# Kernel tuning notes

Hardware: AMD Instinct MI355X
Metric: run time of the kernel (lower is better)

The kernel has to match this reference:

```python
import jax, jax.numpy as jnp
import numpy as np

DIM = 1024
HEADS = 16
DH = DIM // HEADS          # 64
SEQ_LEN = 4096
LATENT = 1024
HIST = SEQ_LEN - LATENT    # 3072
LN_EPS = 1e-5


def setup_inputs() -> dict:
    key = jax.random.key(0)
    ks = jax.random.split(key, 5)
    b = 2
    x = jax.random.normal(ks[0], (b, SEQ_LEN, DIM), dtype=jnp.float32)
    s = 0.02
    Wq = jax.random.normal(ks[1], (DIM, DIM), dtype=jnp.float32) * s
    Wkv = jax.random.normal(ks[2], (DIM, DIM), dtype=jnp.float32) * s
    Wo = jax.random.normal(ks[3], (DIM, DIM), dtype=jnp.float32) * s
    bo = jnp.zeros((DIM,), dtype=jnp.float32)
    gamma = jnp.ones((DH,), dtype=jnp.float32)
    beta = jnp.zeros((DH,), dtype=jnp.float32)
    return {"x": x, "Wq": Wq, "Wkv": Wkv, "Wo": Wo, "bo": bo,
            "gamma": gamma, "beta": beta}


def _rotate_half(t):
    t1, t2 = jnp.split(t, 2, axis=-1)
    return jnp.concatenate([-t2, t1], axis=-1)


def reference(x, Wq, Wkv, Wo, bo, gamma, beta):
    b, n, dim = x.shape
    # projections (nn.Linear: y = x @ W.T), split heads -> (b, h, n, d)
    q = jnp.einsum('bnd,ed->bne', x, Wq).reshape(b, n, HEADS, DH).transpose(0, 2, 1, 3)
    kv = jnp.einsum('bnd,ed->bne', x, Wkv).reshape(b, n, HEADS, DH).transpose(0, 2, 1, 3)

    # layer_num == 0: queries only for the latent segment
    q = q[:, :, HIST:, :]  # (b, h, latent, d)

    # rotary embeddings: concat-style freqs over head dim
    inv_freq = 1.0 / (10000.0 ** (jnp.arange(0, DH, 2, dtype=jnp.float32) / DH))
    freqs = jnp.arange(n, dtype=jnp.float32)[:, None] * inv_freq[None, :]  # (n, DH/2)
    emb = jnp.concatenate([freqs, freqs], axis=-1)  # (n, DH)
    cos, sin = jnp.cos(emb), jnp.sin(emb)
    q = q * cos[HIST:] + _rotate_half(q) * sin[HIST:]
    kv = kv * cos + _rotate_half(kv) * sin

    q = q * (DH ** -0.5)

    # per-kv LayerNorm over head dim
    mu = kv.mean(axis=-1, keepdims=True)
    var = ((kv - mu) ** 2).mean(axis=-1, keepdims=True)
    kvn = (kv - mu) * jax.lax.rsqrt(var + LN_EPS) * gamma + beta

    attn = jnp.einsum('bhid,bhjd->bhij', q, kvn)  # (b, h, latent, n)

    # causal mask only on latent columns: col j (>= HIST) masked if j-HIST > i
    i = jnp.arange(LATENT)[:, None]
    j = jnp.arange(n)[None, :]
    mask = (j - HIST) > i  # false for history columns (j < HIST)
    neg = -jnp.finfo(attn.dtype).max
    attn = jnp.where(mask, neg, attn)

    attn = jax.nn.softmax(attn, axis=-1)
    out = jnp.einsum('bhij,bhjd->bhid', attn, kvn)  # (b, h, latent, d)
    out = out.transpose(0, 2, 1, 3).reshape(b, LATENT, dim)
    return jnp.einsum('bnd,ed->bne', out, Wo) + bo
```

## Files before the change

### kernel.cpp

```cpp
#include <hip/hip_runtime.h>
#include <hip/hip_bf16.h>
#include <cstdint>

#define DIMC 1024
#define HEADS 16
#define DHH 64
#define SEQ 4096
#define LATENT 1024
#define HISTC 3072
#define BATCH 2

typedef __attribute__((ext_vector_type(8))) __bf16 bf16x8;
typedef __attribute__((ext_vector_type(4))) float f32x4;
typedef __attribute__((ext_vector_type(16))) float f32x16;

__global__ void k_convert(const float* __restrict__ in, __bf16* __restrict__ out, int n) {
  int stride = gridDim.x * blockDim.x;
  int nc = n >> 2;
  for (int i = blockIdx.x * blockDim.x + threadIdx.x; i < nc; i += stride) {
    float4 v = reinterpret_cast<const float4*>(in)[i];
    union { __bf16 h[4]; uint64_t u; } p;
    p.h[0] = (__bf16)v.x; p.h[1] = (__bf16)v.y;
    p.h[2] = (__bf16)v.z; p.h[3] = (__bf16)v.w;
    reinterpret_cast<uint64_t*>(out)[i] = p.u;
  }
}

__global__ void k_convert3(const float* __restrict__ a, const float* __restrict__ b,
                           const float* __restrict__ c, __bf16* __restrict__ oa,
                           __bf16* __restrict__ ob, __bf16* __restrict__ oc) {
  int id = blockIdx.x;
  const float* src; __bf16* dst;
  if (id < 512) { src = a; dst = oa; }
  else if (id < 1024) { src = b; dst = ob; id -= 512; }
  else { src = c; dst = oc; id -= 1024; }
#pragma unroll
  for (int k = 0; k < 2; ++k) {
    int idx = id * 512 + k * 256 + threadIdx.x;
    float4 v = reinterpret_cast<const float4*>(src)[idx];
    union { __bf16 h[4]; uint64_t u; } p;
    p.h[0] = (__bf16)v.x; p.h[1] = (__bf16)v.y;
    p.h[2] = (__bf16)v.z; p.h[3] = (__bf16)v.w;
    reinterpret_cast<uint64_t*>(dst)[idx] = p.u;
  }
}

__device__ __forceinline__ void gload16(void* lds, const void* g) {
  __builtin_amdgcn_global_load_lds(
      (const __attribute__((address_space(1))) unsigned int*)g,
      (__attribute__((address_space(3))) unsigned int*)lds, 16, 0, 0);
}

template<int QREMAP, int BIAS>
__launch_bounds__(256)
__global__ void k_gemm(const __bf16* __restrict__ A, const __bf16* __restrict__ Bw,
                       float* __restrict__ C, const float* __restrict__ bias,
                       int M, int N, int K) {
  __shared__ __align__(16) char lds[16384];
  const int t = threadIdx.x;
  const int l = t & 63, w = t >> 6;
  const int wr = w >> 1, wc = w & 1;
  const int m0 = blockIdx.y * 128, n0 = blockIdx.x * 128;
  const int lrow = l & 15, lk = l >> 4;
  f32x4 acc[4][4] = {};

  for (int k0 = 0; k0 < K; k0 += 32) {
    if (k0) __syncthreads();
#pragma unroll
    for (int i = 0; i < 2; ++i) {
      int c = i * 256 + t;
      int row = c >> 2, kc = c & 3;
      int mi = m0 + row;
      if (QREMAP) mi += HISTC + (mi >> 10) * HISTC;
      gload16(lds + c * 16, A + (size_t)mi * K + k0 + kc * 8);
      gload16(lds + 8192 + c * 16, Bw + (size_t)(n0 + row) * K + k0 + kc * 8);
    }
    __syncthreads();
    bf16x8 af[4], bfr[4];
#pragma unroll
    for (int m = 0; m < 4; ++m)
      af[m] = *reinterpret_cast<const bf16x8*>(lds + (wr * 64 + m * 16 + lrow) * 64 + lk * 16);
#pragma unroll
    for (int n = 0; n < 4; ++n)
      bfr[n] = *reinterpret_cast<const bf16x8*>(lds + 8192 + (wc * 64 + n * 16 + lrow) * 64 + lk * 16);
#pragma unroll
    for (int m = 0; m < 4; ++m)
#pragma unroll
      for (int n = 0; n < 4; ++n)
        acc[m][n] = __builtin_amdgcn_mfma_f32_16x16x32_bf16(af[m], bfr[n], acc[m][n], 0, 0, 0);
  }

#pragma unroll
  for (int m = 0; m < 4; ++m)
#pragma unroll
    for (int n = 0; n < 4; ++n)
#pragma unroll
      for (int r = 0; r < 4; ++r) {
        int row = m0 + wr * 64 + m * 16 + (l >> 4) * 4 + r;
        int col = n0 + wc * 64 + n * 16 + (l & 15);
        float v = acc[m][n][r];
        if (BIAS) v += bias[col];
        C[(size_t)row * N + col] = v;
      }
}

__launch_bounds__(256)
__global__ void k_gemmqkv(const __bf16* __restrict__ x16,
                          const __bf16* __restrict__ wkv16,
                          const __bf16* __restrict__ wq16,
                          __bf16* __restrict__ kvn, __bf16* __restrict__ kvnT,
                          __bf16* __restrict__ qb,
                          const float* __restrict__ gamma,
                          const float* __restrict__ beta) {
  __shared__ __align__(16) char lds[16384];
  const int t = threadIdx.x, l = t & 63, w = t >> 6;
  const int wr = w >> 1, wc = w & 1;
  const int by = blockIdx.y;
  const bool isq = by >= 64;
  const int m0 = (isq ? (by - 64) : by) * 128;
  const int n0 = blockIdx.x * 128;
  const __bf16* Bw = isq ? wq16 : wkv16;
  const int lrow = l & 15, lk = l >> 4;
  f32x4 acc[4][4] = {};

  for (int k0 = 0; k0 < 1024; k0 += 32) {
    if (k0) __syncthreads();
#pragma unroll
    for (int i = 0; i < 2; ++i) {
      int c = i * 256 + t;
      int row = c >> 2, kc = c & 3;
      int mi = m0 + row;
      if (isq) mi += HISTC + (mi >> 10) * HISTC;
      gload16(lds + c * 16, x16 + (size_t)mi * 1024 + k0 + kc * 8);
      gload16(lds + 8192 + c * 16, Bw + (size_t)(n0 + row) * 1024 + k0 + kc * 8);
    }
    __syncthreads();
    bf16x8 af[4], bfr[4];
#pragma unroll
    for (int m = 0; m < 4; ++m)
      af[m] = *reinterpret_cast<const bf16x8*>(lds + (wr * 64 + m * 16 + lrow) * 64 + lk * 16);
#pragma unroll
    for (int n = 0; n < 4; ++n)
      bfr[n] = *reinterpret_cast<const bf16x8*>(lds + 8192 + (wc * 64 + n * 16 + lrow) * 64 + lk * 16);
#pragma unroll
    for (int m = 0; m < 4; ++m)
#pragma unroll
      for (int n = 0; n < 4; ++n)
        acc[m][n] = __builtin_amdgcn_mfma_f32_16x16x32_bf16(af[m], bfr[n], acc[m][n], 0, 0, 0);
  }

  const float LG = 0.41524101186f;
  float invf0 = exp2f(-(float)lrow * LG);
  float invf1 = exp2f(-(float)(lrow + 16) * LG);
#pragma unroll
  for (int m = 0; m < 4; ++m)
#pragma unroll
    for (int r = 0; r < 4; ++r) {
      int rl = wr * 64 + m * 16 + lk * 4 + r;
      int pos = isq ? (HISTC + ((m0 + rl) & 1023)) : ((m0 + rl) & 4095);
      float fp = (float)pos;
      float s0, c0, s1, c1;
      sincosf(fp * invf0, &s0, &c0);
      sincosf(fp * invf1, &s1, &c1);
      float a0 = acc[m][0][r], a2 = acc[m][2][r];
      acc[m][0][r] = a0 * c0 - a2 * s0;
      acc[m][2][r] = a2 * c0 + a0 * s0;
      float a1 = acc[m][1][r], a3 = acc[m][3][r];
      acc[m][1][r] = a1 * c1 - a3 * s1;
      acc[m][3][r] = a3 * c1 + a1 * s1;
    }

  const int h = (n0 + wc * 64) >> 6;
  if (!isq) {
    float g4[4], b4[4];
#pragma unroll
    for (int n = 0; n < 4; ++n) { g4[n] = gamma[n * 16 + lrow]; b4[n] = beta[n * 16 + lrow]; }
#pragma unroll
    for (int m = 0; m < 4; ++m)
#pragma unroll
      for (int r = 0; r < 4; ++r) {
        float s1 = acc[m][0][r] + acc[m][1][r] + acc[m][2][r] + acc[m][3][r];
        float s2 = acc[m][0][r] * acc[m][0][r] + acc[m][1][r] * acc[m][1][r] +
                   acc[m][2][r] * acc[m][2][r] + acc[m][3][r] * acc[m][3][r];
#pragma unroll
        for (int mk = 1; mk < 16; mk <<= 1) {
          s1 += __shfl_xor(s1, mk);
          s2 += __shfl_xor(s2, mk);
        }
        float mu = s1 * 0.015625f;
        float var = s2 * 0.015625f - mu * mu;
        float inv = rsqrtf(var + 1e-5f);
#pragma unroll
        for (int n = 0; n < 4; ++n)
          acc[m][n][r] = (acc[m][n][r] - mu) * inv * g4[n] + b4[n];
      }
    const size_t hb = (size_t)((m0 >> 12) * HEADS + h);
#pragma unroll
    for (int m = 0; m < 4; ++m)
#pragma unroll
      for (int r = 0; r < 4; ++r) {
        int pos = (m0 + wr * 64 + m * 16 + lk * 4 + r) & 4095;
#pragma unroll
        for (int n = 0; n < 4; ++n)
          kvn[(hb * SEQ + pos) * DHH + n * 16 + lrow] = (__bf16)acc[m][n][r];
      }
#pragma unroll
    for (int m = 0; m < 4; ++m) {
      int pos0 = (m0 + wr * 64 + m * 16 + lk * 4) & 4095;
      int sp = (pos0 & ~12) | ((pos0 & 4) << 1) | ((pos0 & 8) >> 1);
#pragma unroll
      for (int n = 0; n < 4; ++n) {
        union { __bf16 hh[4]; uint64_t u; } pk;
#pragma unroll
        for (int r = 0; r < 4; ++r) pk.hh[r] = (__bf16)acc[m][n][r];
        *reinterpret_cast<uint64_t*>(kvnT + (hb * DHH + n * 16 + lrow) * SEQ + sp) = pk.u;
      }
    }
  } else {
    const size_t hb = (size_t)((m0 >> 10) * HEADS + h);
#pragma unroll
    for (int m = 0; m < 4; ++m)
#pragma unroll
      for (int r = 0; r < 4; ++r) {
        int qi = (m0 + wr * 64 + m * 16 + lk * 4 + r) & 1023;
#pragma unroll
        for (int n = 0; n < 4; ++n)
          qb[(hb * LATENT + qi) * DHH + n * 16 + lrow] =
              (__bf16)(acc[m][n][r] * 0.18033688011112042f);
      }
  }
}

__device__ __forceinline__ float fexp2(float x) {
#if __has_builtin(__builtin_amdgcn_exp2f)
  return __builtin_amdgcn_exp2f(x);
#else
  return exp2f(x);
#endif
}

__device__ __forceinline__ unsigned pk2(float a, float b) {
  union { __bf16 h[2]; unsigned u; } x;
  x.h[0] = (__bf16)a; x.h[1] = (__bf16)b;
  return x.u;
}

__launch_bounds__(256)
__global__ void k_flash5(const __bf16* __restrict__ qb, const __bf16* __restrict__ kvn,
                         const __bf16* __restrict__ kvnT, __bf16* __restrict__ aout) {
  const int bid = blockIdx.x;
  const int bh = (bid & 7) + 8 * (bid >> 8);
  const int itile = (bid >> 3) & 31;
  const int h = bh & 15, b = bh >> 4;
  const int t = threadIdx.x, l = t & 63, w = t >> 6;
  const int q = l & 31, hi = l >> 5;
  const int iw = itile * 32;
  const int i = iw + q;
  const __bf16* qbase = qb + ((size_t)(b * HEADS + h) * LATENT + iw) * DHH;
  const __bf16* kbase = kvn + (size_t)(b * HEADS + h) * SEQ * DHH;
  const __bf16* vbase = kvnT + (size_t)(b * HEADS + h) * DHH * SEQ;

  __shared__ __align__(16) char smem[4][4352];
  __shared__ float Mlds[4][32];
  __shared__ float Llds[4][32];
  __bf16 (*Vw)[32] = reinterpret_cast<__bf16(*)[32]>(smem[w]);

  bf16x8 qf[4];
#pragma unroll
  for (int c = 0; c < 4; ++c)
    qf[c] = *reinterpret_cast<const bf16x8*>(qbase + (size_t)q * DHH + c * 16 + hi * 8);

  const f32x16 Z = {};
  f32x16 O0 = {}, O1 = {};
  float m_run = -INFINITY, lacc = 0.f;

  const int nt = itile + 97;
  const int t0 = (nt * w) >> 2, t1 = (nt * (w + 1)) >> 2;

  const int srow = l >> 2, scol = l & 3;
  const int wchunk = (scol ^ (srow & 3)) * 8;
  const int sx = q & 3;
  bf16x8 vreg[4], kreg[4];
#pragma unroll
  for (int ii = 0; ii < 4; ++ii)
    vreg[ii] = *reinterpret_cast<const bf16x8*>(
        vbase + (size_t)(ii * 16 + srow) * SEQ + t0 * 32 + scol * 8);
#pragma unroll
  for (int c = 0; c < 4; ++c)
    kreg[c] = *reinterpret_cast<const bf16x8*>(
        kbase + (size_t)(t0 * 32 + q) * DHH + c * 16 + hi * 8);

  for (int tt = t0; tt < t1; ++tt) {
    const int j0 = tt * 32;
    f32x16 S = __builtin_amdgcn_mfma_f32_32x32x16_bf16(kreg[0], qf[0], Z, 0, 0, 0);
#pragma unroll
    for (int c = 1; c < 4; ++c)
      S = __builtin_amdgcn_mfma_f32_32x32x16_bf16(kreg[c], qf[c], S, 0, 0, 0);
#pragma unroll
    for (int ii = 0; ii < 4; ++ii)
      *reinterpret_cast<bf16x8*>(&Vw[ii * 16 + srow][wchunk]) = vreg[ii];
    const int tn = (tt + 1 < t1) ? tt + 1 : tt;
#pragma unroll
    for (int ii = 0; ii < 4; ++ii)
      vreg[ii] = *reinterpret_cast<const bf16x8*>(
          vbase + (size_t)(ii * 16 + srow) * SEQ + tn * 32 + scol * 8);
#pragma unroll
    for (int c = 0; c < 4; ++c)
      kreg[c] = *reinterpret_cast<const bf16x8*>(
          kbase + (size_t)(tn * 32 + q) * DHH + c * 16 + hi * 8);
    if (j0 + 31 > iw + HISTC) {
#pragma unroll
      for (int r = 0; r < 16; ++r) {
        int j = j0 + (r & 3) + 8 * (r >> 2) + 4 * hi;
        if (j > i + HISTC) S[r] = -1e30f;
      }
    }
    float u1 = fmaxf(fmaxf(S[0], S[1]), S[2]);
    float u2 = fmaxf(fmaxf(S[3], S[4]), S[5]);
    float u3 = fmaxf(fmaxf(S[6], S[7]), S[8]);
    float u4 = fmaxf(fmaxf(S[9], S[10]), S[11]);
    float u5 = fmaxf(fmaxf(S[12], S[13]), S[14]);
    float pm = fmaxf(fmaxf(fmaxf(u1, u2), u3), fmaxf(fmaxf(u4, u5), S[15]));
    if (__any(pm > m_run + 8.0f)) {
      pm = fmaxf(pm, __shfl_xor(pm, 32));
      float mn = fmaxf(m_run, pm);
      float sc = fexp2(m_run - mn);
      m_run = mn;
      lacc *= sc;
#pragma unroll
      for (int r = 0; r < 16; ++r) { O0[r] *= sc; O1[r] *= sc; }
    }
    float p[16];
#pragma unroll
    for (int r = 0; r < 16; ++r) p[r] = fexp2(S[r] - m_run);
    float s8[8];
#pragma unroll
    for (int r = 0; r < 8; ++r) s8[r] = p[r] + p[r + 8];
    float s4_0 = s8[0] + s8[4], s4_1 = s8[1] + s8[5];
    float s4_2 = s8[2] + s8[6], s4_3 = s8[3] + s8[7];
    lacc += (s4_0 + s4_1) + (s4_2 + s4_3);
    union { unsigned u[4]; bf16x8 v; } pf0, pf1;
    pf0.u[0] = pk2(p[0], p[1]);   pf0.u[1] = pk2(p[2], p[3]);
    pf0.u[2] = pk2(p[4], p[5]);   pf0.u[3] = pk2(p[6], p[7]);
    pf1.u[0] = pk2(p[8], p[9]);   pf1.u[1] = pk2(p[10], p[11]);
    pf1.u[2] = pk2(p[12], p[13]); pf1.u[3] = pk2(p[14], p[15]);
    {
      bf16x8 va00 = *reinterpret_cast<const bf16x8*>(&Vw[q][(hi ^ sx) * 8]);
      bf16x8 va01 = *reinterpret_cast<const bf16x8*>(&Vw[q][((2 + hi) ^ sx) * 8]);
      bf16x8 va10 = *reinterpret_cast<const bf16x8*>(&Vw[32 + q][(hi ^ sx) * 8]);
      bf16x8 va11 = *reinterpret_cast<const bf16x8*>(&Vw[32 + q][((2 + hi) ^ sx) * 8]);
      O0 = __builtin_amdgcn_mfma_f32_32x32x16_bf16(va00, pf0.v, O0, 0, 0, 0);
      O0 = __builtin_amdgcn_mfma_f32_32x32x16_bf16(va01, pf1.v, O0, 0, 0, 0);
      O1 = __builtin_amdgcn_mfma_f32_32x32x16_bf16(va10, pf0.v, O1, 0, 0, 0);
      O1 = __builtin_amdgcn_mfma_f32_32x32x16_bf16(va11, pf1.v, O1, 0, 0, 0);
    }
  }
  float l_run = lacc + __shfl_xor(lacc, 32);

  float (*Ow)[33] = reinterpret_cast<float(*)[33]>(smem[w]);
  if (hi == 0) { Mlds[w][q] = m_run; Llds[w][q] = l_run; }
#pragma unroll
  for (int r = 0; r < 16; ++r)
    Ow[q][(r & 3) + 8 * (r >> 2) + 4 * hi] = O0[r];
  __syncthreads();
  const int mi = t >> 3, dl = (t & 7) * 4;
  float m0v = Mlds[0][mi], m1v = Mlds[1][mi], m2v = Mlds[2][mi], m3v = Mlds[3][mi];
  float mm = fmaxf(fmaxf(m0v, m1v), fmaxf(m2v, m3v));
  float sc0 = fexp2(m0v - mm), sc1 = fexp2(m1v - mm);
  float sc2 = fexp2(m2v - mm), sc3 = fexp2(m3v - mm);
  float ll = Llds[0][mi] * sc0 + Llds[1][mi] * sc1 + Llds[2][mi] * sc2 + Llds[3][mi] * sc3;
  float inv = 1.f / ll;
  __bf16* orow = aout + ((size_t)(b * LATENT) + iw + mi) * DIMC + h * DHH;
  {
    float(*O0p)[33] = reinterpret_cast<float(*)[33]>(smem[0]);
    float(*O1p)[33] = reinterpret_cast<float(*)[33]>(smem[1]);
    float(*O2p)[33] = reinterpret_cast<float(*)[33]>(smem[2]);
    float(*O3p)[33] = reinterpret_cast<float(*)[33]>(smem[3]);
    union { __bf16 hh[4]; uint2 u2; } pkv;
#pragma unroll
    for (int e = 0; e < 4; ++e) {
      float o = O0p[mi][dl + e] * sc0 + O1p[mi][dl + e] * sc1 +
                O2p[mi][dl + e] * sc2 + O3p[mi][dl + e] * sc3;
      pkv.hh[e] = (__bf16)(o * inv);
    }
    *reinterpret_cast<uint2*>(orow + dl) = pkv.u2;
  }
  __syncthreads();
#pragma unroll
  for (int r = 0; r < 16; ++r)
    Ow[q][(r & 3) + 8 * (r >> 2) + 4 * hi] = O1[r];
  __syncthreads();
  {
    float(*O0p)[33] = reinterpret_cast<float(*)[33]>(smem[0]);
    float(*O1p)[33] = reinterpret_cast<float(*)[33]>(smem[1]);
    float(*O2p)[33] = reinterpret_cast<float(*)[33]>(smem[2]);
    float(*O3p)[33] = reinterpret_cast<float(*)[33]>(smem[3]);
    union { __bf16 hh[4]; uint2 u2; } pkv;
#pragma unroll
    for (int e = 0; e < 4; ++e) {
      float o = O0p[mi][dl + e] * sc0 + O1p[mi][dl + e] * sc1 +
                O2p[mi][dl + e] * sc2 + O3p[mi][dl + e] * sc3;
      pkv.hh[e] = (__bf16)(o * inv);
    }
    *reinterpret_cast<uint2*>(orow + 32 + dl) = pkv.u2;
  }
}

extern "C" void kernel_launch(void* const* d_in, const int* in_sizes, int n_in,
                              void* d_out, int out_size, void* d_ws, size_t ws_size,
                              hipStream_t stream) {
  const float* x = (const float*)d_in[0];
  const float* Wq = (const float*)d_in[1];
  const float* Wkv = (const float*)d_in[2];
  const float* Wo = (const float*)d_in[3];
  const float* bo = (const float*)d_in[4];
  const float* gamma = (const float*)d_in[5];
  const float* beta = (const float*)d_in[6];

  char* ws = (char*)d_ws;
  size_t o = 0;
  __bf16* x16 = (__bf16*)(ws + o);  o += (size_t)BATCH * SEQ * DIMC * 2;
  __bf16* wq16 = (__bf16*)(ws + o); o += (size_t)DIMC * DIMC * 2;
  __bf16* wkv16 = (__bf16*)(ws + o); o += (size_t)DIMC * DIMC * 2;
  __bf16* wo16 = (__bf16*)(ws + o); o += (size_t)DIMC * DIMC * 2;
  __bf16* kvn = (__bf16*)(ws + o);  o += (size_t)BATCH * HEADS * SEQ * DHH * 2;
  __bf16* kvnT = (__bf16*)(ws + o); o += (size_t)BATCH * HEADS * SEQ * DHH * 2;
  __bf16* qb = (__bf16*)(ws + o);   o += (size_t)BATCH * HEADS * LATENT * DHH * 2;
  __bf16* aout = (__bf16*)(ws + o); o += (size_t)BATCH * LATENT * DIMC * 2;

  k_convert<<<2048, 256, 0, stream>>>(x, x16, BATCH * SEQ * DIMC);
  k_convert3<<<1536, 256, 0, stream>>>(Wq, Wkv, Wo, wq16, wkv16, wo16);
  k_gemmqkv<<<dim3(8, 80), 256, 0, stream>>>(x16, wkv16, wq16, kvn, kvnT, qb, gamma, beta);
  k_flash5<<<1024, 256, 0, stream>>>(qb, kvn, kvnT, aout);
  k_gemm<0, 1><<<dim3(8, 16), 256, 0, stream>>>(aout, wo16, (float*)d_out, bo, 2048, 1024, 1024);
}
```

Baseline: 173.4 us.

## Split flash attention over KV halves, precompute rotary table, fuse conversion kernels

Each query tile's key range is now split across two blocks (8 slices total), with itile reversed in the second half for load balance. Partial outputs with their running max and sum are written to an fp32 buffer, and a new merge kernel combines them into bf16. The three conversion kernels are fused into one prep kernel that also builds a cos/sin table, which the QKV GEMM reads instead of calling sincosf per element. The GEMM grids are also linearized so M varies fastest within a column. The extra partial buffer, the additional launch and the table loads add memory traffic in exchange for more parallelism and less transcendental work.

```diff
diff --git a/kernel.cpp b/kernel.cpp
--- a/kernel.cpp
+++ b/kernel.cpp
@@ -14,34 +14,45 @@
 typedef __attribute__((ext_vector_type(4))) float f32x4;
 typedef __attribute__((ext_vector_type(16))) float f32x16;
 
-__global__ void k_convert(const float* __restrict__ in, __bf16* __restrict__ out, int n) {
-  int stride = gridDim.x * blockDim.x;
-  int nc = n >> 2;
-  for (int i = blockIdx.x * blockDim.x + threadIdx.x; i < nc; i += stride) {
-    float4 v = reinterpret_cast<const float4*>(in)[i];
-    union { __bf16 h[4]; uint64_t u; } p;
-    p.h[0] = (__bf16)v.x; p.h[1] = (__bf16)v.y;
-    p.h[2] = (__bf16)v.z; p.h[3] = (__bf16)v.w;
-    reinterpret_cast<uint64_t*>(out)[i] = p.u;
-  }
-}
-
-__global__ void k_convert3(const float* __restrict__ a, const float* __restrict__ b,
-                           const float* __restrict__ c, __bf16* __restrict__ oa,
-                           __bf16* __restrict__ ob, __bf16* __restrict__ oc) {
-  int id = blockIdx.x;
-  const float* src; __bf16* dst;
-  if (id < 512) { src = a; dst = oa; }
-  else if (id < 1024) { src = b; dst = ob; id -= 512; }
-  else { src = c; dst = oc; id -= 1024; }
-#pragma unroll
-  for (int k = 0; k < 2; ++k) {
-    int idx = id * 512 + k * 256 + threadIdx.x;
-    float4 v = reinterpret_cast<const float4*>(src)[idx];
-    union { __bf16 h[4]; uint64_t u; } p;
-    p.h[0] = (__bf16)v.x; p.h[1] = (__bf16)v.y;
-    p.h[2] = (__bf16)v.z; p.h[3] = (__bf16)v.w;
-    reinterpret_cast<uint64_t*>(dst)[idx] = p.u;
+__global__ void k_prep(const float* __restrict__ x, const float* __restrict__ Wq,
+                       const float* __restrict__ Wkv, const float* __restrict__ Wo,
+                       __bf16* __restrict__ x16, __bf16* __restrict__ wq16,
+                       __bf16* __restrict__ wkv16, __bf16* __restrict__ wo16,
+                       float2* __restrict__ cs) {
+  int bidx = blockIdx.x;
+  if (bidx < 2048) {
+    int base = bidx * 256 + threadIdx.x;
+#pragma unroll
+    for (int k = 0; k < 4; ++k) {
+      int i = base + k * 524288;
+      float4 v = reinterpret_cast<const float4*>(x)[i];
+      union { __bf16 h[4]; uint64_t u; } p;
+      p.h[0] = (__bf16)v.x; p.h[1] = (__bf16)v.y;
+      p.h[2] = (__bf16)v.z; p.h[3] = (__bf16)v.w;
+      reinterpret_cast<uint64_t*>(x16)[i] = p.u;
+    }
+  } else if (bidx < 3584) {
+    int id = bidx - 2048;
+    const float* src; __bf16* dst;
+    if (id < 512) { src = Wq; dst = wq16; }
+    else if (id < 1024) { src = Wkv; dst = wkv16; id -= 512; }
+    else { src = Wo; dst = wo16; id -= 1024; }
+#pragma unroll
+    for (int k = 0; k < 2; ++k) {
+      int idx = id * 512 + k * 256 + threadIdx.x;
+      float4 v = reinterpret_cast<const float4*>(src)[idx];
+      union { __bf16 h[4]; uint64_t u; } p;
+      p.h[0] = (__bf16)v.x; p.h[1] = (__bf16)v.y;
+      p.h[2] = (__bf16)v.z; p.h[3] = (__bf16)v.w;
+      reinterpret_cast<uint64_t*>(dst)[idx] = p.u;
+    }
+  } else {
+    int idx = (bidx - 3584) * 256 + threadIdx.x;
+    int pos = idx >> 5, f = idx & 31;
+    float invf = exp2f(-(float)f * 0.41524101186f);
+    float s, c;
+    sincosf((float)pos * invf, &s, &c);
+    cs[idx] = make_float2(c, s);
   }
 }
 
@@ -51,7 +62,7 @@
       (__attribute__((address_space(3))) unsigned int*)lds, 16, 0, 0);
 }
 
-template<int QREMAP, int BIAS>
+template<int BIAS>
 __launch_bounds__(256)
 __global__ void k_gemm(const __bf16* __restrict__ A, const __bf16* __restrict__ Bw,
                        float* __restrict__ C, const float* __restrict__ bias,
@@ -60,7 +71,8 @@
   const int t = threadIdx.x;
   const int l = t & 63, w = t >> 6;
   const int wr = w >> 1, wc = w & 1;
-  const int m0 = blockIdx.y * 128, n0 = blockIdx.x * 128;
+  const int mblocks = M >> 7;
+  const int m0 = (blockIdx.x % mblocks) * 128, n0 = (blockIdx.x / mblocks) * 128;
   const int lrow = l & 15, lk = l >> 4;
   f32x4 acc[4][4] = {};
 
@@ -70,9 +82,7 @@
     for (int i = 0; i < 2; ++i) {
       int c = i * 256 + t;
       int row = c >> 2, kc = c & 3;
-      int mi = m0 + row;
-      if (QREMAP) mi += HISTC + (mi >> 10) * HISTC;
-      gload16(lds + c * 16, A + (size_t)mi * K + k0 + kc * 8);
+      gload16(lds + c * 16, A + (size_t)(m0 + row) * K + k0 + kc * 8);
       gload16(lds + 8192 + c * 16, Bw + (size_t)(n0 + row) * K + k0 + kc * 8);
     }
     __syncthreads();
@@ -111,14 +121,15 @@
                           __bf16* __restrict__ kvn, __bf16* __restrict__ kvnT,
                           __bf16* __restrict__ qb,
                           const float* __restrict__ gamma,
-                          const float* __restrict__ beta) {
+                          const float* __restrict__ beta,
+                          const float2* __restrict__ cstab) {
   __shared__ __align__(16) char lds[16384];
   const int t = threadIdx.x, l = t & 63, w = t >> 6;
   const int wr = w >> 1, wc = w & 1;
-  const int by = blockIdx.y;
+  const int by = blockIdx.x % 80;
   const bool isq = by >= 64;
   const int m0 = (isq ? (by - 64) : by) * 128;
-  const int n0 = blockIdx.x * 128;
+  const int n0 = (blockIdx.x / 80) * 128;
   const __bf16* Bw = isq ? wq16 : wkv16;
   const int lrow = l & 15, lk = l >> 4;
   f32x4 acc[4][4] = {};
@@ -149,25 +160,20 @@
         acc[m][n] = __builtin_amdgcn_mfma_f32_16x16x32_bf16(af[m], bfr[n], acc[m][n], 0, 0, 0);
   }
 
-  const float LG = 0.41524101186f;
-  float invf0 = exp2f(-(float)lrow * LG);
-  float invf1 = exp2f(-(float)(lrow + 16) * LG);
 #pragma unroll
   for (int m = 0; m < 4; ++m)
 #pragma unroll
     for (int r = 0; r < 4; ++r) {
       int rl = wr * 64 + m * 16 + lk * 4 + r;
       int pos = isq ? (HISTC + ((m0 + rl) & 1023)) : ((m0 + rl) & 4095);
-      float fp = (float)pos;
-      float s0, c0, s1, c1;
-      sincosf(fp * invf0, &s0, &c0);
-      sincosf(fp * invf1, &s1, &c1);
+      float2 cs0 = cstab[pos * 32 + lrow];
+      float2 cs1 = cstab[pos * 32 + 16 + lrow];
       float a0 = acc[m][0][r], a2 = acc[m][2][r];
-      acc[m][0][r] = a0 * c0 - a2 * s0;
-      acc[m][2][r] = a2 * c0 + a0 * s0;
+      acc[m][0][r] = a0 * cs0.x - a2 * cs0.y;
+      acc[m][2][r] = a2 * cs0.x + a0 * cs0.y;
       float a1 = acc[m][1][r], a3 = acc[m][3][r];
-      acc[m][1][r] = a1 * c1 - a3 * s1;
-      acc[m][3][r] = a3 * c1 + a1 * s1;
+      acc[m][1][r] = a1 * cs1.x - a3 * cs1.y;
+      acc[m][3][r] = a3 * cs1.x + a1 * cs1.y;
     }
 
   const int h = (n0 + wc * 64) >> 6;
@@ -246,11 +252,14 @@
 }
 
 __launch_bounds__(256)
-__global__ void k_flash5(const __bf16* __restrict__ qb, const __bf16* __restrict__ kvn,
-                         const __bf16* __restrict__ kvnT, __bf16* __restrict__ aout) {
+__global__ void k_flash8(const __bf16* __restrict__ qb, const __bf16* __restrict__ kvn,
+                         const __bf16* __restrict__ kvnT, float* __restrict__ part) {
   const int bid = blockIdx.x;
-  const int bh = (bid & 7) + 8 * (bid >> 8);
-  const int itile = (bid >> 3) & 31;
+  const int grp = bid >> 9;
+  const int jh = (bid >> 8) & 1;
+  const int bh = (bid & 7) + 8 * grp;
+  int itile = (bid >> 3) & 31;
+  if (jh) itile = 31 - itile;
   const int h = bh & 15, b = bh >> 4;
   const int t = threadIdx.x, l = t & 63, w = t >> 6;
   const int q = l & 31, hi = l >> 5;
@@ -275,7 +284,8 @@
   float m_run = -INFINITY, lacc = 0.f;
 
   const int nt = itile + 97;
-  const int t0 = (nt * w) >> 2, t1 = (nt * (w + 1)) >> 2;
+  const int s = jh * 4 + w;
+  const int t0 = (nt * s) >> 3, t1 = (nt * (s + 1)) >> 3;
 
   const int srow = l >> 2, scol = l & 3;
   const int wchunk = (scol ^ (srow & 3)) * 8;
@@ -293,9 +303,9 @@
   for (int tt = t0; tt < t1; ++tt) {
     const int j0 = tt * 32;
     f32x16 S = __builtin_amdgcn_mfma_f32_32x32x16_bf16(kreg[0], qf[0], Z, 0, 0, 0);
-#pragma unroll
-    for (int c = 1; c < 4; ++c)
-      S = __builtin_amdgcn_mfma_f32_32x32x16_bf16(kreg[c], qf[c], S, 0, 0, 0);
+    S = __builtin_amdgcn_mfma_f32_32x32x16_bf16(kreg[1], qf[1], S, 0, 0, 0);
+    S = __builtin_amdgcn_mfma_f32_32x32x16_bf16(kreg[2], qf[2], S, 0, 0, 0);
+    S = __builtin_amdgcn_mfma_f32_32x32x16_bf16(kreg[3], qf[3], S, 0, 0, 0);
 #pragma unroll
     for (int ii = 0; ii < 4; ++ii)
       *reinterpret_cast<bf16x8*>(&Vw[ii * 16 + srow][wchunk]) = vreg[ii];
@@ -336,9 +346,7 @@
     float s8[8];
 #pragma unroll
     for (int r = 0; r < 8; ++r) s8[r] = p[r] + p[r + 8];
-    float s4_0 = s8[0] + s8[4], s4_1 = s8[1] + s8[5];
-    float s4_2 = s8[2] + s8[6], s4_3 = s8[3] + s8[7];
-    lacc += (s4_0 + s4_1) + (s4_2 + s4_3);
+    lacc += ((s8[0] + s8[4]) + (s8[1] + s8[5])) + ((s8[2] + s8[6]) + (s8[3] + s8[7]));
     union { unsigned u[4]; bf16x8 v; } pf0, pf1;
     pf0.u[0] = pk2(p[0], p[1]);   pf0.u[1] = pk2(p[2], p[3]);
     pf0.u[2] = pk2(p[4], p[5]);   pf0.u[3] = pk2(p[6], p[7]);
@@ -357,6 +365,8 @@
   }
   float l_run = lacc + __shfl_xor(lacc, 32);
 
+  const int pidx = (bh * 32 + itile) * 2 + jh;
+  float* prow_base = part + (size_t)pidx * 32 * 68;
   float (*Ow)[33] = reinterpret_cast<float(*)[33]>(smem[w]);
   if (hi == 0) { Mlds[w][q] = m_run; Llds[w][q] = l_run; }
 #pragma unroll
@@ -369,21 +379,19 @@
   float sc0 = fexp2(m0v - mm), sc1 = fexp2(m1v - mm);
   float sc2 = fexp2(m2v - mm), sc3 = fexp2(m3v - mm);
   float ll = Llds[0][mi] * sc0 + Llds[1][mi] * sc1 + Llds[2][mi] * sc2 + Llds[3][mi] * sc3;
-  float inv = 1.f / ll;
-  __bf16* orow = aout + ((size_t)(b * LATENT) + iw + mi) * DIMC + h * DHH;
+  float* prow = prow_base + (size_t)mi * 68;
   {
     float(*O0p)[33] = reinterpret_cast<float(*)[33]>(smem[0]);
     float(*O1p)[33] = reinterpret_cast<float(*)[33]>(smem[1]);
     float(*O2p)[33] = reinterpret_cast<float(*)[33]>(smem[2]);
     float(*O3p)[33] = reinterpret_cast<float(*)[33]>(smem[3]);
-    union { __bf16 hh[4]; uint2 u2; } pkv;
-#pragma unroll
-    for (int e = 0; e < 4; ++e) {
-      float o = O0p[mi][dl + e] * sc0 + O1p[mi][dl + e] * sc1 +
-                O2p[mi][dl + e] * sc2 + O3p[mi][dl + e] * sc3;
-      pkv.hh[e] = (__bf16)(o * inv);
-    }
-    *reinterpret_cast<uint2*>(orow + dl) = pkv.u2;
+    float4 o;
+    o.x = O0p[mi][dl + 0] * sc0 + O1p[mi][dl + 0] * sc1 + O2p[mi][dl + 0] * sc2 + O3p[mi][dl + 0] * sc3;
+    o.y = O0p[mi][dl + 1] * sc0 + O1p[mi][dl + 1] * sc1 + O2p[mi][dl + 1] * sc2 + O3p[mi][dl + 1] * sc3;
+    o.z = O0p[mi][dl + 2] * sc0 + O1p[mi][dl + 2] * sc1 + O2p[mi][dl + 2] * sc2 + O3p[mi][dl + 2] * sc3;
+    o.w = O0p[mi][dl + 3] * sc0 + O1p[mi][dl + 3] * sc1 + O2p[mi][dl + 3] * sc2 + O3p[mi][dl + 3] * sc3;
+    *reinterpret_cast<float4*>(prow + dl) = o;
+    if ((t & 7) == 0) { prow[64] = mm; prow[65] = ll; }
   }
   __syncthreads();
 #pragma unroll
@@ -395,15 +403,32 @@
     float(*O1p)[33] = reinterpret_cast<float(*)[33]>(smem[1]);
     float(*O2p)[33] = reinterpret_cast<float(*)[33]>(smem[2]);
     float(*O3p)[33] = reinterpret_cast<float(*)[33]>(smem[3]);
-    union { __bf16 hh[4]; uint2 u2; } pkv;
-#pragma unroll
-    for (int e = 0; e < 4; ++e) {
-      float o = O0p[mi][dl + e] * sc0 + O1p[mi][dl + e] * sc1 +
-                O2p[mi][dl + e] * sc2 + O3p[mi][dl + e] * sc3;
-      pkv.hh[e] = (__bf16)(o * inv);
-    }
-    *reinterpret_cast<uint2*>(orow + 32 + dl) = pkv.u2;
-  }
+    float4 o;
+    o.x = O0p[mi][dl + 0] * sc0 + O1p[mi][dl + 0] * sc1 + O2p[mi][dl + 0] * sc2 + O3p[mi][dl + 0] * sc3;
+    o.y = O0p[mi][dl + 1] * sc0 + O1p[mi][dl + 1] * sc1 + O2p[mi][dl + 1] * sc2 + O3p[mi][dl + 1] * sc3;
+    o.z = O0p[mi][dl + 2] * sc0 + O1p[mi][dl + 2] * sc1 + O2p[mi][dl + 2] * sc2 + O3p[mi][dl + 2] * sc3;
+    o.w = O0p[mi][dl + 3] * sc0 + O1p[mi][dl + 3] * sc1 + O2p[mi][dl + 3] * sc2 + O3p[mi][dl + 3] * sc3;
+    *reinterpret_cast<float4*>(prow + 32 + dl) = o;
+  }
+}
+
+__global__ void k_fmerge(const float* __restrict__ part, __bf16* __restrict__ aout) {
+  const int u = blockIdx.x;
+  const int bh = u >> 5, itile = u & 31;
+  const int b = bh >> 4, h = bh & 15, iw = itile * 32;
+  const int t = threadIdx.x;
+  const int mi = t >> 3, d0 = (t & 7) * 8;
+  const float* p0 = part + ((size_t)(u * 2 + 0) * 32 + mi) * 68;
+  const float* p1 = part + ((size_t)(u * 2 + 1) * 32 + mi) * 68;
+  float m0 = p0[64], l0 = p0[65], m1 = p1[64], l1 = p1[65];
+  float mm = fmaxf(m0, m1);
+  float sc0 = fexp2(m0 - mm), sc1 = fexp2(m1 - mm);
+  float inv = 1.f / (l0 * sc0 + l1 * sc1);
+  union { __bf16 hh[8]; uint4 u4; } pk;
+#pragma unroll
+  for (int e = 0; e < 8; ++e)
+    pk.hh[e] = (__bf16)((p0[d0 + e] * sc0 + p1[d0 + e] * sc1) * inv);
+  *reinterpret_cast<uint4*>(aout + ((size_t)(b * LATENT) + iw + mi) * DIMC + h * DHH + d0) = pk.u4;
 }
 
 extern "C" void kernel_launch(void* const* d_in, const int* in_sizes, int n_in,
@@ -423,14 +448,16 @@
   __bf16* wq16 = (__bf16*)(ws + o); o += (size_t)DIMC * DIMC * 2;
   __bf16* wkv16 = (__bf16*)(ws + o); o += (size_t)DIMC * DIMC * 2;
   __bf16* wo16 = (__bf16*)(ws + o); o += (size_t)DIMC * DIMC * 2;
+  float2* cstab = (float2*)(ws + o); o += (size_t)SEQ * 32 * 8;
   __bf16* kvn = (__bf16*)(ws + o);  o += (size_t)BATCH * HEADS * SEQ * DHH * 2;
   __bf16* kvnT = (__bf16*)(ws + o); o += (size_t)BATCH * HEADS * SEQ * DHH * 2;
   __bf16* qb = (__bf16*)(ws + o);   o += (size_t)BATCH * HEADS * LATENT * DHH * 2;
   __bf16* aout = (__bf16*)(ws + o); o += (size_t)BATCH * LATENT * DIMC * 2;
-
-  k_convert<<<2048, 256, 0, stream>>>(x, x16, BATCH * SEQ * DIMC);
-  k_convert3<<<1536, 256, 0, stream>>>(Wq, Wkv, Wo, wq16, wkv16, wo16);
-  k_gemmqkv<<<dim3(8, 80), 256, 0, stream>>>(x16, wkv16, wq16, kvn, kvnT, qb, gamma, beta);
-  k_flash5<<<1024, 256, 0, stream>>>(qb, kvn, kvnT, aout);
-  k_gemm<0, 1><<<dim3(8, 16), 256, 0, stream>>>(aout, wo16, (float*)d_out, bo, 2048, 1024, 1024);
-}
+  float* part = (float*)(ws + o);   o += (size_t)2048 * 32 * 68 * 4;
+
+  k_prep<<<4096, 256, 0, stream>>>(x, Wq, Wkv, Wo, x16, wq16, wkv16, wo16, cstab);
+  k_gemmqkv<<<640, 256, 0, stream>>>(x16, wkv16, wq16, kvn, kvnT, qb, gamma, beta, cstab);
+  k_flash8<<<2048, 256, 0, stream>>>(qb, kvn, kvnT, part);
+  k_fmerge<<<1024, 256, 0, stream>>>(part, aout);
+  k_gemm<1><<<128, 256, 0, stream>>>(aout, wo16, (float*)d_out, bo, 2048, 1024, 1024);
+}
```

Result: no change. 175.8 us (+1.4%).
